# Optimization experiments

Hardware: AMD Instinct MI355X
Metric: run time of the kernel (lower is better)

Reference implementation:

```python
import jax, jax.numpy as jnp
import numpy as np

TAU = 0.07
EPS = 1e-8  # matches torch F.cosine_similarity eps


def _normalize(x):
    # torch cosine_similarity clamps norm at eps
    n = jnp.sqrt(jnp.sum(x * x, axis=-1, keepdims=True))
    return x / jnp.maximum(n, EPS)


def setup_inputs() -> dict:
    key = jax.random.key(0)
    k1, k2 = jax.random.split(key)
    N, D = 8192, 512
    z_i = jax.random.normal(k1, (N, D), dtype=jnp.float32)
    z_j = jax.random.normal(k2, (N, D), dtype=jnp.float32)
    return {"z_i": z_i, "z_j": z_j}


def reference(z_i, z_j):
    N = z_i.shape[0]
    zi_n = _normalize(z_i)
    zj_n = _normalize(z_j)
    # fused: cosine sim via normalized matmul instead of [N,N,D] repeat
    sim = jnp.einsum("nd,md->nm", zi_n, zj_n) / TAU  # [N, N]
    pos_sim = jnp.diagonal(sim)                      # [N]
    neg_sim = jnp.where(jnp.eye(N, dtype=bool), -jnp.inf, sim)
    # -log(exp(pos)/sum(exp(neg))) == -pos + logsumexp(neg) (stable form, same math)
    lse_row = jax.nn.logsumexp(neg_sim, axis=1)  # sum over dim=-1
    lse_col = jax.nn.logsumexp(neg_sim, axis=0)  # sum over dim=0
    loss_e2t = jnp.mean(lse_row - pos_sim)
    loss_t2e = jnp.mean(lse_col - pos_sim)
    loss = (loss_e2t + loss_t2e) / 2
    return jnp.stack([loss, loss_e2t, loss_t2e])
```

## Files before the change

kernel.cpp:

```cpp
#include <hip/hip_runtime.h>
#include <hip/hip_fp8.h>

#define NROWS 8192
#define DDIM  512
#define INV_TAU 14.285714285714286f

typedef float f32x16 __attribute__((ext_vector_type(16)));
typedef long  longx2 __attribute__((ext_vector_type(2)));

__device__ static inline unsigned char f2e4(float f) {
  __hip_fp8_e4m3 h(f); return (unsigned char)h.__x;
}
__device__ static inline float e4f(unsigned char b) {
  __hip_fp8_e4m3 h; h.__x = b; return (float)h;
}


__global__ __launch_bounds__(256) void norm_kernel(
    const float* __restrict__ zi, const float* __restrict__ zj,
    unsigned char* __restrict__ ziN, unsigned char* __restrict__ zjN) {
  int rid = blockIdx.x * 4 + (threadIdx.x >> 6);
  int lane = threadIdx.x & 63;
  const float* src;
  unsigned char* dstbase;
  int row;
  if (rid < NROWS) { src = zi + (size_t)rid * DDIM; dstbase = ziN; row = rid; }
  else             { src = zj + (size_t)(rid - NROWS) * DDIM; dstbase = zjN; row = rid - NROWS; }
  float4 v0 = *(const float4*)(src + lane * 8);
  float4 v1 = *(const float4*)(src + lane * 8 + 4);
  float ss = v0.x*v0.x + v0.y*v0.y + v0.z*v0.z + v0.w*v0.w
           + v1.x*v1.x + v1.y*v1.y + v1.z*v1.z + v1.w*v1.w;
  #pragma unroll
  for (int off = 1; off < 64; off <<= 1) ss += __shfl_xor(ss, off);
  float scale = 1.0f / fmaxf(sqrtf(ss), 1e-8f);
  unsigned long long w = 0;
  w |= (unsigned long long)f2e4(v0.x * scale);
  w |= (unsigned long long)f2e4(v0.y * scale) << 8;
  w |= (unsigned long long)f2e4(v0.z * scale) << 16;
  w |= (unsigned long long)f2e4(v0.w * scale) << 24;
  w |= (unsigned long long)f2e4(v1.x * scale) << 32;
  w |= (unsigned long long)f2e4(v1.y * scale) << 40;
  w |= (unsigned long long)f2e4(v1.z * scale) << 48;
  w |= (unsigned long long)f2e4(v1.w * scale) << 56;
  int p = row >> 5, r = row & 31, c = lane;
  *(unsigned long long*)(dstbase + (size_t)p * 16384 + (c >> 2) * 1024 +
                         ((c & 1) * 32 + r) * 16 + ((c >> 1) & 1) * 8) = w;
}

__global__ __launch_bounds__(256) void zero_kernel(float* __restrict__ p) {
  p[blockIdx.x * 256 + threadIdx.x] = 0.0f;
}

__global__ __launch_bounds__(256) void pos_kernel(
    const unsigned char* __restrict__ ziN, const unsigned char* __restrict__ zjN,
    float* __restrict__ pos) {
  int row = blockIdx.x * 4 + (threadIdx.x >> 6);
  int lane = threadIdx.x & 63;
  int p = row >> 5, r = row & 31, c = lane;
  size_t off = (size_t)p * 16384 + (c >> 2) * 1024 + ((c & 1) * 32 + r) * 16 + ((c >> 1) & 1) * 8;
  unsigned long long a8 = *(const unsigned long long*)(ziN + off);
  unsigned long long b8 = *(const unsigned long long*)(zjN + off);
  float s = 0.0f;
  #pragma unroll
  for (int j = 0; j < 8; ++j)
    s += e4f((unsigned char)(a8 >> (8 * j))) * e4f((unsigned char)(b8 >> (8 * j)));
  #pragma unroll
  for (int off2 = 1; off2 < 64; off2 <<= 1) s += __shfl_xor(s, off2);
  if (lane == 0) pos[row] = s * INV_TAU;
}

__global__ __launch_bounds__(256, 4) void sim_reg(
    const unsigned char* __restrict__ Ap, const unsigned char* __restrict__ Bp,
    float* __restrict__ row_sum, float* __restrict__ col_sum) {
  const int tid  = threadIdx.x;
  const int lane = tid & 63;
  const int wid  = tid >> 6;
  const int wr   = wid >> 1, wc = wid & 1;
  const int cl   = lane & 31;
  const int h    = lane >> 5;
  const int orig = blockIdx.x;
  const int xcd  = orig & 7;
  const int seq  = orig >> 3;
  const int by   = xcd * 8 + (seq & 7);
  const int bx   = seq >> 3;
  const int brow = by * 128, bcol = bx * 128;

  f32x16 acc[2][2] = {};

  const unsigned char* pa0 = Ap + (size_t)(by * 4 + wr * 2) * 16384 + lane * 16;
  const unsigned char* pa1 = pa0 + 16384;
  const unsigned char* pb0 = Bp + (size_t)(bx * 4 + wc * 2) * 16384 + lane * 16;
  const unsigned char* pb1 = pb0 + 16384;

  longx2 a0 = *(const longx2*)pa0;
  longx2 a1 = *(const longx2*)pa1;
  longx2 b0 = *(const longx2*)pb0;
  longx2 b1 = *(const longx2*)pb1;

  #pragma unroll 4
  for (int u = 0; u < 16; ++u) {
    const int un = ((u + 1) & 15) * 1024;
    longx2 na0 = *(const longx2*)(pa0 + un);
    longx2 na1 = *(const longx2*)(pa1 + un);
    longx2 nb0 = *(const longx2*)(pb0 + un);
    longx2 nb1 = *(const longx2*)(pb1 + un);
    acc[0][0] = __builtin_amdgcn_mfma_f32_32x32x16_fp8_fp8(a0[0], b0[0], acc[0][0], 0, 0, 0);
    acc[0][1] = __builtin_amdgcn_mfma_f32_32x32x16_fp8_fp8(a0[0], b1[0], acc[0][1], 0, 0, 0);
    acc[1][0] = __builtin_amdgcn_mfma_f32_32x32x16_fp8_fp8(a1[0], b0[0], acc[1][0], 0, 0, 0);
    acc[1][1] = __builtin_amdgcn_mfma_f32_32x32x16_fp8_fp8(a1[0], b1[0], acc[1][1], 0, 0, 0);
    acc[0][0] = __builtin_amdgcn_mfma_f32_32x32x16_fp8_fp8(a0[1], b0[1], acc[0][0], 0, 0, 0);
    acc[0][1] = __builtin_amdgcn_mfma_f32_32x32x16_fp8_fp8(a0[1], b1[1], acc[0][1], 0, 0, 0);
    acc[1][0] = __builtin_amdgcn_mfma_f32_32x32x16_fp8_fp8(a1[1], b0[1], acc[1][0], 0, 0, 0);
    acc[1][1] = __builtin_amdgcn_mfma_f32_32x32x16_fp8_fp8(a1[1], b1[1], acc[1][1], 0, 0, 0);
    a0 = na0; a1 = na1; b0 = nb0; b1 = nb1;
  }

  const float Cc = INV_TAU * 1.4426950408889634f;
  #pragma unroll
  for (int mf = 0; mf < 2; ++mf)
    #pragma unroll
    for (int nf = 0; nf < 2; ++nf) {
      int gj = bcol + wc * 64 + nf * 32 + cl;
      #pragma unroll
      for (int reg = 0; reg < 16; ++reg) {
        int gi = brow + wr * 64 + mf * 32 + (reg & 3) + 8 * (reg >> 2) + 4 * h;
        float e = exp2f((acc[mf][nf][reg] - 1.0f) * Cc);
        acc[mf][nf][reg] = (gi == gj) ? 0.0f : e;
      }
    }
  #pragma unroll
  for (int nf = 0; nf < 2; ++nf) {
    float cs = 0.0f;
    #pragma unroll
    for (int mf = 0; mf < 2; ++mf)
      #pragma unroll
      for (int reg = 0; reg < 16; ++reg) cs += acc[mf][nf][reg];
    cs += __shfl_xor(cs, 32);
    if (lane < 32) atomicAdd(&col_sum[bcol + wc * 64 + nf * 32 + lane], cs);
  }
  #pragma unroll
  for (int mf = 0; mf < 2; ++mf)
    #pragma unroll
    for (int reg = 0; reg < 16; ++reg) {
      float rs = acc[mf][0][reg] + acc[mf][1][reg];
      rs += __shfl_xor(rs, 1);
      rs += __shfl_xor(rs, 2);
      rs += __shfl_xor(rs, 4);
      rs += __shfl_xor(rs, 8);
      rs += __shfl_xor(rs, 16);
      if (cl == 0)
        atomicAdd(&row_sum[brow + wr * 64 + mf * 32 + (reg & 3) + 8 * (reg >> 2) + 4 * h], rs);
    }
}

__global__ __launch_bounds__(256) void finalize_kernel(
    const float* __restrict__ row_sum, const float* __restrict__ col_sum,
    const float* __restrict__ pos, float* __restrict__ out) {
  __shared__ float sA[4], sB[4];
  float sa = 0.0f, sb = 0.0f;
  for (int i = threadIdx.x; i < NROWS; i += 256) {
    float p = pos[i];
    sa += (INV_TAU + __logf(row_sum[i])) - p;
    sb += (INV_TAU + __logf(col_sum[i])) - p;
  }
  #pragma unroll
  for (int off = 1; off < 64; off <<= 1) {
    sa += __shfl_xor(sa, off);
    sb += __shfl_xor(sb, off);
  }
  if ((threadIdx.x & 63) == 0) { sA[threadIdx.x >> 6] = sa; sB[threadIdx.x >> 6] = sb; }
  __syncthreads();
  if (threadIdx.x == 0) {
    float ta = sA[0] + sA[1] + sA[2] + sA[3];
    float tb = sB[0] + sB[1] + sB[2] + sB[3];
    float e2t = ta / (float)NROWS;
    float t2e = tb / (float)NROWS;
    out[0] = 0.5f * (e2t + t2e);
    out[1] = e2t;
    out[2] = t2e;
  }
}

extern "C" void kernel_launch(void* const* d_in, const int* in_sizes, int n_in,
                              void* d_out, int out_size, void* d_ws, size_t ws_size,
                              hipStream_t stream) {
  const float* z_i = (const float*)d_in[0];
  const float* z_j = (const float*)d_in[1];
  float* out = (float*)d_out;
  char* ws = (char*)d_ws;
  unsigned char* ziN = (unsigned char*)ws;
  unsigned char* zjN = (unsigned char*)(ws + 4194304);
  float* row_sum = (float*)(ws + 8388608);
  float* col_sum = row_sum + NROWS;
  float* pos     = col_sum + NROWS;

  norm_kernel<<<4096, 256, 0, stream>>>(z_i, z_j, ziN, zjN);
  zero_kernel<<<64, 256, 0, stream>>>(row_sum);
  pos_kernel<<<2048, 256, 0, stream>>>(ziN, zjN, pos);
  sim_reg<<<4096, 256, 0, stream>>>(ziN, zjN, row_sum, col_sum);
  finalize_kernel<<<1, 256, 0, stream>>>(row_sum, col_sum, pos, out);
}
```

Baseline: 113.8 us.

## Stage fp8 GEMM operands through double-buffered LDS with direct global-to-LDS loads

The similarity kernel now copies each 32-row A/B panel once per block into shared memory using global_load_lds, double-buffered across 8 k-stages, and waves read their fragments from LDS. Previously each panel was loaded from global memory by two waves, so this halves cache traffic. In exchange it adds per-stage barriers, LDS reads and 32KB of LDS per block, which may constrain occupancy.

```diff
diff --git a/kernel.cpp b/kernel.cpp
--- a/kernel.cpp
+++ b/kernel.cpp
@@ -13,6 +13,12 @@
 }
 __device__ static inline float e4f(unsigned char b) {
   __hip_fp8_e4m3 h; h.__x = b; return (float)h;
+}
+
+__device__ static inline void load_lds16(const void* g, void* l) {
+  __builtin_amdgcn_global_load_lds(
+      (const __attribute__((address_space(1))) void*)g,
+      (__attribute__((address_space(3))) void*)l, 16, 0, 0);
 }
 
 
@@ -69,9 +75,11 @@
   if (lane == 0) pos[row] = s * INV_TAU;
 }
 
-__global__ __launch_bounds__(256, 4) void sim_reg(
+__global__ __launch_bounds__(256, 4) void sim_lds(
     const unsigned char* __restrict__ Ap, const unsigned char* __restrict__ Bp,
     float* __restrict__ row_sum, float* __restrict__ col_sum) {
+  __shared__ __align__(16) unsigned char lds[32768];
+
   const int tid  = threadIdx.x;
   const int lane = tid & 63;
   const int wid  = tid >> 6;
@@ -87,32 +95,53 @@
 
   f32x16 acc[2][2] = {};
 
-  const unsigned char* pa0 = Ap + (size_t)(by * 4 + wr * 2) * 16384 + lane * 16;
-  const unsigned char* pa1 = pa0 + 16384;
-  const unsigned char* pb0 = Bp + (size_t)(bx * 4 + wc * 2) * 16384 + lane * 16;
-  const unsigned char* pb1 = pb0 + 16384;
-
-  longx2 a0 = *(const longx2*)pa0;
-  longx2 a1 = *(const longx2*)pa1;
-  longx2 b0 = *(const longx2*)pb0;
-  longx2 b1 = *(const longx2*)pb1;
-
-  #pragma unroll 4
-  for (int u = 0; u < 16; ++u) {
-    const int un = ((u + 1) & 15) * 1024;
-    longx2 na0 = *(const longx2*)(pa0 + un);
-    longx2 na1 = *(const longx2*)(pa1 + un);
-    longx2 nb0 = *(const longx2*)(pb0 + un);
-    longx2 nb1 = *(const longx2*)(pb1 + un);
-    acc[0][0] = __builtin_amdgcn_mfma_f32_32x32x16_fp8_fp8(a0[0], b0[0], acc[0][0], 0, 0, 0);
-    acc[0][1] = __builtin_amdgcn_mfma_f32_32x32x16_fp8_fp8(a0[0], b1[0], acc[0][1], 0, 0, 0);
-    acc[1][0] = __builtin_amdgcn_mfma_f32_32x32x16_fp8_fp8(a1[0], b0[0], acc[1][0], 0, 0, 0);
-    acc[1][1] = __builtin_amdgcn_mfma_f32_32x32x16_fp8_fp8(a1[0], b1[0], acc[1][1], 0, 0, 0);
-    acc[0][0] = __builtin_amdgcn_mfma_f32_32x32x16_fp8_fp8(a0[1], b0[1], acc[0][0], 0, 0, 0);
-    acc[0][1] = __builtin_amdgcn_mfma_f32_32x32x16_fp8_fp8(a0[1], b1[1], acc[0][1], 0, 0, 0);
-    acc[1][0] = __builtin_amdgcn_mfma_f32_32x32x16_fp8_fp8(a1[1], b0[1], acc[1][0], 0, 0, 0);
-    acc[1][1] = __builtin_amdgcn_mfma_f32_32x32x16_fp8_fp8(a1[1], b1[1], acc[1][1], 0, 0, 0);
-    a0 = na0; a1 = na1; b0 = nb0; b1 = nb1;
+  const unsigned char* gA = Ap + (size_t)(by * 4 + wid) * 16384 + lane * 16;
+  const unsigned char* gB = Bp + (size_t)(bx * 4 + wid) * 16384 + lane * 16;
+  char* ldsA = (char*)lds + wid * 2048 + lane * 16;
+  char* ldsB = (char*)lds + 8192 + wid * 2048 + lane * 16;
+
+  auto stage = [&](int t) {
+    const int buf = (t & 1) * 16384;
+    const int u0  = (2 * t) << 10;
+    load_lds16(gA + u0,        ldsA + buf);
+    load_lds16(gA + u0 + 1024, ldsA + buf + 1024);
+    load_lds16(gB + u0,        ldsB + buf);
+    load_lds16(gB + u0 + 1024, ldsB + buf + 1024);
+  };
+
+  const char* rA = (const char*)lds + wr * 2 * 2048 + lane * 16;
+  const char* rB = (const char*)lds + 8192 + wc * 2 * 2048 + lane * 16;
+
+  stage(0);
+
+  #pragma unroll
+  for (int t = 0; t < 8; ++t) {
+    if (t < 7) {
+      stage(t + 1);
+      asm volatile("s_waitcnt vmcnt(4)" ::: "memory");
+    } else {
+      asm volatile("s_waitcnt vmcnt(0)" ::: "memory");
+    }
+    __builtin_amdgcn_s_barrier();
+    const int buf = (t & 1) * 16384;
+    longx2 a[2][2], b[2][2];
+    #pragma unroll
+    for (int i = 0; i < 2; ++i)
+      #pragma unroll
+      for (int kk = 0; kk < 2; ++kk) {
+        a[i][kk] = *(const longx2*)(rA + buf + i * 2048 + kk * 1024);
+        b[i][kk] = *(const longx2*)(rB + buf + i * 2048 + kk * 1024);
+      }
+    #pragma unroll
+    for (int kk = 0; kk < 2; ++kk)
+      #pragma unroll
+      for (int kb = 0; kb < 2; ++kb) {
+        acc[0][0] = __builtin_amdgcn_mfma_f32_32x32x16_fp8_fp8(a[0][kk][kb], b[0][kk][kb], acc[0][0], 0, 0, 0);
+        acc[0][1] = __builtin_amdgcn_mfma_f32_32x32x16_fp8_fp8(a[0][kk][kb], b[1][kk][kb], acc[0][1], 0, 0, 0);
+        acc[1][0] = __builtin_amdgcn_mfma_f32_32x32x16_fp8_fp8(a[1][kk][kb], b[0][kk][kb], acc[1][0], 0, 0, 0);
+        acc[1][1] = __builtin_amdgcn_mfma_f32_32x32x16_fp8_fp8(a[1][kk][kb], b[1][kk][kb], acc[1][1], 0, 0, 0);
+      }
+    __builtin_amdgcn_s_barrier();
   }
 
   const float Cc = INV_TAU * 1.4426950408889634f;
@@ -197,6 +226,6 @@
   norm_kernel<<<4096, 256, 0, stream>>>(z_i, z_j, ziN, zjN);
   zero_kernel<<<64, 256, 0, stream>>>(row_sum);
   pos_kernel<<<2048, 256, 0, stream>>>(ziN, zjN, pos);
-  sim_reg<<<4096, 256, 0, stream>>>(ziN, zjN, row_sum, col_sum);
+  sim_lds<<<4096, 256, 0, stream>>>(ziN, zjN, row_sum, col_sum);
   finalize_kernel<<<1, 256, 0, stream>>>(row_sum, col_sum, pos, out);
 }
```

New measurement: 103.1 us. 1.1x faster.
